# Kernel optimization log

Hardware: AMD Instinct MI355X
Metric: run time of the kernel (lower is better)

Reference implementation:

```python
import jax, jax.numpy as jnp
import numpy as np

N = 50000      # nodes
E = 512000     # directed edges (module assumes 2nd half is reverse of 1st half)
DIN = 128      # in_channels
EDIM = 128     # edge_dim (== in_channels, required by HypergraphConv branch)
H = 4          # heads
C = 32         # out_channels per head
EPS = 1e-5     # BatchNorm eps


def _segment_softmax(logits, seg, num):
    # PyG-style scatter softmax over segments (stable: subtract per-segment max)
    m = jax.ops.segment_max(logits, seg, num_segments=num)
    m = jnp.where(jnp.isfinite(m), m, 0.0)
    ex = jnp.exp(logits - m[seg])
    s = jax.ops.segment_sum(ex, seg, num_segments=num)
    return ex / (s[seg] + 1e-16)


def setup_inputs() -> dict:
    key = jax.random.key(0)
    ks = jax.random.split(key, 24)

    def lin(k, fin, fout):
        return (jax.random.normal(k, (fin, fout), jnp.float32) / np.sqrt(fin)).astype(jnp.float32)

    return {
        "x": jax.random.normal(ks[0], (N, DIN), jnp.float32),
        "edge_attr": jax.random.normal(ks[1], (E, EDIM), jnp.float32),
        # TransformerConv params
        "Wq": lin(ks[2], DIN, H * C), "bq": 0.01 * jax.random.normal(ks[3], (H * C,), jnp.float32),
        "Wk": lin(ks[4], DIN, H * C), "bk": 0.01 * jax.random.normal(ks[5], (H * C,), jnp.float32),
        "Wv": lin(ks[6], DIN, H * C), "bv": 0.01 * jax.random.normal(ks[7], (H * C,), jnp.float32),
        "We2": lin(ks[8], EDIM, H * C), "be2": 0.01 * jax.random.normal(ks[9], (H * C,), jnp.float32),
        "We3": lin(ks[10], EDIM, H * C), "be3": 0.01 * jax.random.normal(ks[11], (H * C,), jnp.float32),
        "Wcon": lin(ks[12], H * C, C),
        # BatchNorm1d params
        "bn_w": 1.0 + 0.01 * jax.random.normal(ks[13], (C,), jnp.float32),
        "bn_b": 0.01 * jax.random.normal(ks[14], (C,), jnp.float32),
        # HypergraphConv params (use_attention=False, heads=1)
        "Wh1": lin(ks[15], EDIM, C),
        "Wh2": lin(ks[16], DIN, C),
        "bh": jnp.zeros((C,), jnp.float32),
        # integer inputs
        "edge_index": jax.random.randint(ks[17], (2, E), 0, N, dtype=jnp.int32),
        "batch": jnp.zeros((N,), jnp.int32),
    }


def reference(x, edge_attr, Wq, bq, Wk, bk, Wv, bv, We2, be2, We3, be3, Wcon,
              bn_w, bn_b, Wh1, Wh2, bh, edge_index, batch):
    n = x.shape[0]
    e = edge_index.shape[1]
    src, dst = edge_index[0], edge_index[1]

    # ---- TransformerConv (edge-attention message passing) ----
    q = (x @ Wq + bq).reshape(n, H, C)
    k = (x @ Wk + bk).reshape(n, H, C)
    v = (x @ Wv + bv).reshape(n, H, C)
    ea2 = (edge_attr @ We2 + be2).reshape(e, H, C)
    ea3 = (edge_attr @ We3 + be3).reshape(e, H, C)
    qi, kj, vj = q[dst], k[src], v[src]          # gather per edge: [E,H,C]
    scale = 1.0 / np.sqrt(C)
    a1 = _segment_softmax((qi * kj).sum(-1) * scale, dst, n)    # [E,H]
    a2 = _segment_softmax((qi * ea2).sum(-1) * scale, dst, n)   # [E,H]
    msg = (vj * a1[..., None] + ea3 * a2[..., None]).reshape(e, H * C) @ Wcon  # [E,C]
    x_gat = jax.ops.segment_sum(msg, dst, num_segments=n)       # [N,C]

    # BatchNorm1d (training-mode batch stats, biased var) + exact GELU
    mu = x_gat.mean(0)
    var = ((x_gat - mu) ** 2).mean(0)
    x_gat = jax.nn.gelu(bn_w * (x_gat - mu) * jax.lax.rsqrt(var + EPS) + bn_b,
                        approximate=False)

    # ---- DHT dual hypergraph + HypergraphConv (no attention) ----
    e2 = e // 2
    ei = edge_index[:, :e2]           # first half of (bidirectional) edges
    ea = edge_attr[:e2]
    he_node = jnp.repeat(jnp.arange(e2, dtype=jnp.int32), 2)  # dual-node (edge) ids, [2*E2]
    he_edge = ei.T.reshape(-1)                                 # hyperedge (orig node) ids, [2*E2]

    xh = ea @ Wh1      # lin(edge_attr): [E2,C] (heads=1)
    attr = x @ Wh2     # lin2(x):        [N,C]

    ones = jnp.ones((2 * e2,), jnp.float32)
    deg_d = jax.ops.segment_sum(ones, he_node, num_segments=e2)   # D (== 2 per edge)
    Dinv = jnp.where(deg_d > 0, 1.0 / deg_d, 0.0)
    deg_b = jax.ops.segment_sum(ones, he_edge, num_segments=n)    # B (node degree)
    Binv = jnp.where(deg_b > 0, 1.0 / deg_b, 0.0)

    # propagate 1: dual-node -> hyperedge, norm B, then add hyperedge_attr
    o1 = jax.ops.segment_sum(Binv[he_edge][:, None] * xh[he_node],
                             he_edge, num_segments=n) + attr       # [N,C]
    # propagate 2 (flipped): hyperedge -> dual-node, norm D, add bias
    edge_attr2 = jax.ops.segment_sum(Dinv[he_node][:, None] * o1[he_edge],
                                     he_node, num_segments=e2) + bh  # [E2,C]

    return (x_gat, edge_attr2)
```

## Files before the change

kernel.cpp:

```cpp
#include <hip/hip_runtime.h>
#include <math.h>

#define NN 50000
#define NE 512000
#define NE2 256000
#define SCALE 0.17677669529663687f
#define EPSV 1e-5f
#define CHUNK 128000

#define OFF_Q      0UL
#define OFF_K      6400000UL
#define OFF_V      12800000UL
#define OFF_ATTR   0UL
#define OFF_O1     1600000UL
#define OFF_XGAT   3200000UL
#define OFF_O1ACC  4800000UL
#define OFF_DEGB   6400000UL
#define OFF_STATS  6450000UL
#define OFF_EX1    19200000UL
#define OFF_EX2    21248000UL
#define OFF_CC     23296000UL
#define OFF_S1     31488000UL
#define OFF_S2     31688000UL
#define OFF_XH     19200000UL
#define OFF_AGG    31888000UL
#define OFF_WBT    38288000UL
#define OFF_BIASB  38304384UL

typedef __attribute__((ext_vector_type(8))) short bf16x8;
typedef __attribute__((ext_vector_type(8))) unsigned short us8;
typedef __attribute__((ext_vector_type(4))) float f32x4;

__device__ __forceinline__ unsigned short f2bf(float f) {
    unsigned int u = __float_as_uint(f);
    unsigned int r = (u + 0x7FFFu + ((u >> 16) & 1u)) >> 16;
    return (unsigned short)r;
}
__device__ __forceinline__ float bf2f(unsigned short u) {
    return __uint_as_float(((unsigned int)u) << 16);
}

__global__ void pack_w(const float* __restrict__ We2, const float* __restrict__ be2,
                       const float* __restrict__ We3, const float* __restrict__ be3,
                       unsigned short* __restrict__ WbT, float* __restrict__ biasb) {
    const int idx = blockIdx.x * 256 + threadIdx.x;
    if (idx < 32768) {
        const int j = idx >> 7;
        const int k = idx & 127;
        const float w = (j < 128) ? We2[k * 128 + j] : We3[k * 128 + (j - 128)];
        WbT[idx] = f2bf(w);
    } else if (idx < 33024) {
        const int jj = idx - 32768;
        biasb[jj] = (jj < 128) ? be2[jj] : be3[jj - 128];
    }
}

__global__ __launch_bounds__(256)
void gemm_ea(const float* __restrict__ A, const unsigned short* __restrict__ WbT,
             const float* __restrict__ biasb, unsigned short* __restrict__ Cc, int half) {
    __shared__ unsigned short As[128 * 72];
    __shared__ unsigned short Bs[128 * 72];
    const int tid = threadIdx.x;
    const int wave = tid >> 6;
    const int lane = tid & 63;
    const int quad = lane >> 4;
    const int l16 = lane & 15;
    const int m0 = (wave & 1) * 64;
    const int n0 = (wave >> 1) * 64;
    const size_t r0 = (size_t)blockIdx.x * 128;

    f32x4 acc[4][4];
    #pragma unroll
    for (int i = 0; i < 4; i++)
        #pragma unroll
        for (int j = 0; j < 4; j++) acc[i][j] = (f32x4){0.f, 0.f, 0.f, 0.f};

    for (int kh = 0; kh < 2; kh++) {
        #pragma unroll
        for (int i = 0; i < 8; i++) {
            const int q = tid + 256 * i;
            const int row = q >> 4;
            const int c4 = q & 15;
            const float4 a4 = *(const float4*)(A + (r0 + row) * 128 + kh * 64 + c4 * 4);
            ushort4 b4;
            b4.x = f2bf(a4.x); b4.y = f2bf(a4.y); b4.z = f2bf(a4.z); b4.w = f2bf(a4.w);
            *(ushort4*)(&As[row * 72 + c4 * 4]) = b4;
        }
        {
            const int n = tid >> 1;
            const int koff = (tid & 1) * 32;
            const unsigned short* src = WbT + (size_t)(half * 128 + n) * 128 + kh * 64 + koff;
            #pragma unroll
            for (int u = 0; u < 4; u++) {
                *(us8*)(&Bs[n * 72 + koff + 8 * u]) = *(const us8*)(src + 8 * u);
            }
        }
        __syncthreads();
        #pragma unroll
        for (int kc = 0; kc < 64; kc += 32) {
            bf16x8 af[4], bf[4];
            #pragma unroll
            for (int i = 0; i < 4; i++)
                af[i] = *(const bf16x8*)(&As[(m0 + 16 * i + l16) * 72 + kc + quad * 8]);
            #pragma unroll
            for (int j = 0; j < 4; j++)
                bf[j] = *(const bf16x8*)(&Bs[(n0 + 16 * j + l16) * 72 + kc + quad * 8]);
            #pragma unroll
            for (int i = 0; i < 4; i++)
                #pragma unroll
                for (int j = 0; j < 4; j++)
                    acc[i][j] = __builtin_amdgcn_mfma_f32_16x16x32_bf16(af[i], bf[j], acc[i][j], 0, 0, 0);
        }
        __syncthreads();
    }
    #pragma unroll
    for (int j = 0; j < 4; j++) {
        const int col = n0 + 16 * j + l16;
        const float bcol = biasb[half * 128 + col];
        #pragma unroll
        for (int i = 0; i < 4; i++) {
            #pragma unroll
            for (int r = 0; r < 4; r++) {
                const int row = m0 + 16 * i + quad * 4 + r;
                Cc[(r0 + row) * 128 + col] = f2bf(acc[i][j][r] + bcol);
            }
        }
    }
}

__global__ void qkv_kernel(const float* __restrict__ x,
                           const float* __restrict__ Wq, const float* __restrict__ bq,
                           const float* __restrict__ Wk, const float* __restrict__ bk,
                           const float* __restrict__ Wv, const float* __restrict__ bv,
                           float* __restrict__ q, float* __restrict__ k, float* __restrict__ v) {
    __shared__ float xs[8 * 128];
    const int tid = threadIdx.x;
    const int j = tid & 127;
    const int g = tid >> 7;
    const size_t n0 = (size_t)blockIdx.x * 8;
    ((float4*)xs)[tid] = ((const float4*)(x + n0 * 128))[tid];
    __syncthreads();
    float aq[4] = {0,0,0,0}, ak[4] = {0,0,0,0}, av[4] = {0,0,0,0};
    #pragma unroll 4
    for (int d = 0; d < 128; d++) {
        const float wq = Wq[d*128 + j];
        const float wk = Wk[d*128 + j];
        const float wv = Wv[d*128 + j];
        #pragma unroll
        for (int r = 0; r < 4; r++) {
            const float xv = xs[(g + 2*r)*128 + d];
            aq[r] += xv * wq; ak[r] += xv * wk; av[r] += xv * wv;
        }
    }
    const float bqv = bq[j], bkv = bk[j], bvv = bv[j];
    #pragma unroll
    for (int r = 0; r < 4; r++) {
        const size_t n = n0 + g + 2*r;
        q[n*128 + j] = aq[r] + bqv;
        k[n*128 + j] = ak[r] + bkv;
        v[n*128 + j] = av[r] + bvv;
    }
}

__global__ void pass1(const int* __restrict__ eidx,
                      const float* __restrict__ q, const float* __restrict__ k,
                      const unsigned short* __restrict__ Cc, long e_base,
                      float* __restrict__ ex1, float* __restrict__ ex2,
                      float* __restrict__ s1, float* __restrict__ s2) {
    const size_t e = (size_t)e_base + blockIdx.x * 4 + (threadIdx.x >> 6);
    const int lane = threadIdx.x & 63;
    const int src = eidx[e];
    const int dst = eidx[NE + e];
    const float2 qv = ((const float2*)(q + (size_t)dst * 128))[lane];
    const float2 kv = ((const float2*)(k + (size_t)src * 128))[lane];
    const unsigned int cc = ((const unsigned int*)(Cc + (e - e_base) * 128))[lane];
    const float ea2a = bf2f((unsigned short)(cc & 0xFFFF));
    const float ea2b = bf2f((unsigned short)(cc >> 16));
    float p1 = qv.x * kv.x + qv.y * kv.y;
    float p2 = qv.x * ea2a + qv.y * ea2b;
    #pragma unroll
    for (int off = 8; off > 0; off >>= 1) {
        p1 += __shfl_down(p1, off, 16);
        p2 += __shfl_down(p2, off, 16);
    }
    if ((lane & 15) == 0) {
        const int h = lane >> 4;
        const float v1 = __expf(p1 * SCALE);
        const float v2 = __expf(p2 * SCALE);
        ex1[e * 4 + h] = v1;
        ex2[e * 4 + h] = v2;
        atomicAdd(&s1[(size_t)dst * 4 + h], v1);
        atomicAdd(&s2[(size_t)dst * 4 + h], v2);
    }
}

__global__ void pass2(const int* __restrict__ eidx,
                      const float* __restrict__ v,
                      const unsigned short* __restrict__ Cc, long e_base,
                      const float* __restrict__ ex1, const float* __restrict__ ex2,
                      const float* __restrict__ s1, const float* __restrict__ s2,
                      float* __restrict__ agg) {
    const size_t e = (size_t)e_base + blockIdx.x * 4 + (threadIdx.x >> 6);
    const int lane = threadIdx.x & 63;
    const int src = eidx[e];
    const int dst = eidx[NE + e];
    float a1l = 0.f, a2l = 0.f;
    if (lane < 4) {
        a1l = ex1[e * 4 + lane] / (s1[(size_t)dst * 4 + lane] + 1e-16f);
        a2l = ex2[e * 4 + lane] / (s2[(size_t)dst * 4 + lane] + 1e-16f);
    }
    const int h1 = lane >> 5;
    const int h2 = 2 + (lane >> 5);
    const float a1c1 = __shfl(a1l, h1), a1c2 = __shfl(a1l, h2);
    const float a2c1 = __shfl(a2l, h1), a2c2 = __shfl(a2l, h2);
    const float vv1 = v[(size_t)src * 128 + lane];
    const float vv2 = v[(size_t)src * 128 + lane + 64];
    const float e31 = bf2f(Cc[(e - e_base) * 128 + lane]);
    const float e32 = bf2f(Cc[(e - e_base) * 128 + lane + 64]);
    atomicAdd(&agg[(size_t)dst * 128 + lane],      a1c1 * vv1 + a2c1 * e31);
    atomicAdd(&agg[(size_t)dst * 128 + lane + 64], a1c2 * vv2 + a2c2 * e32);
}

__global__ void gemm_d128_o32(const float* __restrict__ A, const float* __restrict__ W,
                              float* __restrict__ out) {
    __shared__ float as[8 * 128];
    const int tid = threadIdx.x;
    const int p = tid & 31;
    const int mm = tid >> 5;
    const size_t m0 = (size_t)blockIdx.x * 8;
    ((float4*)as)[tid] = ((const float4*)(A + m0 * 128))[tid];
    __syncthreads();
    float c0 = 0.f, c1 = 0.f, c2 = 0.f, c3 = 0.f;
    const float4* as4 = (const float4*)as;
    #pragma unroll 8
    for (int i = 0; i < 32; i++) {
        const float4 a4 = as4[mm*32 + i];
        c0 += a4.x * W[(4*i+0)*32 + p];
        c1 += a4.y * W[(4*i+1)*32 + p];
        c2 += a4.z * W[(4*i+2)*32 + p];
        c3 += a4.w * W[(4*i+3)*32 + p];
    }
    out[(m0 + mm)*32 + p] = (c0 + c1) + (c2 + c3);
}

__global__ void bn_stats(const float* __restrict__ xg, float* __restrict__ stats) {
    __shared__ float ls[256], lss[256];
    const int tid = threadIdx.x;
    float s = 0.f, ss = 0.f;
    for (size_t i = (size_t)blockIdx.x*256 + tid; i < (size_t)NN*32; i += (size_t)gridDim.x*256) {
        const float val = xg[i];
        s += val; ss += val * val;
    }
    ls[tid] = s; lss[tid] = ss;
    __syncthreads();
    if (tid < 32) {
        float as_ = 0.f, ass = 0.f;
        #pragma unroll
        for (int w = 0; w < 8; w++) { as_ += ls[tid + 32*w]; ass += lss[tid + 32*w]; }
        atomicAdd(&stats[tid], as_);
        atomicAdd(&stats[32 + tid], ass);
    }
}

__global__ void bn_gelu(const float* __restrict__ xg, const float* __restrict__ stats,
                        const float* __restrict__ bnw, const float* __restrict__ bnb,
                        float* __restrict__ out) {
    const size_t i = (size_t)blockIdx.x * 256 + threadIdx.x;
    const int c = i & 31;
    const float mu = stats[c] * (1.0f / NN);
    const float var = stats[32 + c] * (1.0f / NN) - mu * mu;
    const float xn = bnw[c] * (xg[i] - mu) * rsqrtf(var + EPSV) + bnb[c];
    out[i] = 0.5f * xn * (1.0f + erff(xn * 0.70710678118654752f));
}

__global__ void hyper_scatter(const float* __restrict__ xh, const int* __restrict__ eidx,
                              float* __restrict__ o1acc, float* __restrict__ degb) {
    const int tid = threadIdx.x;
    const int c = tid & 31;
    const size_t i = (size_t)blockIdx.x * 8 + (tid >> 5);
    const int src = eidx[i];
    const int dst = eidx[NE + i];
    const float xv = xh[i*32 + c];
    atomicAdd(&o1acc[(size_t)src*32 + c], xv);
    atomicAdd(&o1acc[(size_t)dst*32 + c], xv);
    if (c == 0) {
        atomicAdd(&degb[src], 1.0f);
        atomicAdd(&degb[dst], 1.0f);
    }
}

__global__ void o1_finalize(const float* __restrict__ o1acc, const float* __restrict__ degb,
                            const float* __restrict__ attr, float* __restrict__ o1) {
    const size_t i = (size_t)blockIdx.x * 256 + threadIdx.x;
    const int n = (int)(i >> 5);
    const float d = degb[n];
    const float binv = d > 0.f ? 1.0f / d : 0.0f;
    o1[i] = o1acc[i] * binv + attr[i];
}

__global__ void edge_out(const float* __restrict__ o1, const int* __restrict__ eidx,
                         const float* __restrict__ bh, float* __restrict__ out2) {
    const size_t idx = (size_t)blockIdx.x * 256 + threadIdx.x;
    const size_t i = idx >> 5;
    const int c = (int)(idx & 31);
    const int src = eidx[i];
    const int dst = eidx[NE + i];
    out2[idx] = 0.5f * (o1[(size_t)src*32 + c] + o1[(size_t)dst*32 + c]) + bh[c];
}

extern "C" void kernel_launch(void* const* d_in, const int* in_sizes, int n_in,
                              void* d_out, int out_size, void* d_ws, size_t ws_size,
                              hipStream_t stream) {
    const float* x    = (const float*)d_in[0];
    const float* eatt = (const float*)d_in[1];
    const float* Wq   = (const float*)d_in[2];
    const float* bq   = (const float*)d_in[3];
    const float* Wk   = (const float*)d_in[4];
    const float* bk   = (const float*)d_in[5];
    const float* Wv   = (const float*)d_in[6];
    const float* bv   = (const float*)d_in[7];
    const float* We2  = (const float*)d_in[8];
    const float* be2  = (const float*)d_in[9];
    const float* We3  = (const float*)d_in[10];
    const float* be3  = (const float*)d_in[11];
    const float* Wcon = (const float*)d_in[12];
    const float* bnw  = (const float*)d_in[13];
    const float* bnb  = (const float*)d_in[14];
    const float* Wh1  = (const float*)d_in[15];
    const float* Wh2  = (const float*)d_in[16];
    const float* bh   = (const float*)d_in[17];
    const int*   eidx = (const int*)d_in[18];

    float* ws = (float*)d_ws;
    float* q     = ws + OFF_Q;
    float* k     = ws + OFF_K;
    float* v     = ws + OFF_V;
    float* ex1   = ws + OFF_EX1;
    float* ex2   = ws + OFF_EX2;
    unsigned short* Cc = (unsigned short*)(ws + OFF_CC);
    float* s1    = ws + OFF_S1;
    float* s2    = ws + OFF_S2;
    float* agg   = ws + OFF_AGG;
    unsigned short* WbT = (unsigned short*)(ws + OFF_WBT);
    float* biasb = ws + OFF_BIASB;
    float* attr  = ws + OFF_ATTR;
    float* o1    = ws + OFF_O1;
    float* xgat  = ws + OFF_XGAT;
    float* o1acc = ws + OFF_O1ACC;
    float* degb  = ws + OFF_DEGB;
    float* stats = ws + OFF_STATS;
    float* xh    = ws + OFF_XH;
    float* out0  = (float*)d_out;
    float* out1  = (float*)d_out + (size_t)NN * 32;

    hipMemsetAsync(ws + OFF_S1, 0, (38288000UL - OFF_S1) * sizeof(float), stream);

    pack_w<<<129, 256, 0, stream>>>(We2, be2, We3, be3, WbT, biasb);
    qkv_kernel<<<6250, 256, 0, stream>>>(x, Wq, bq, Wk, bk, Wv, bv, q, k, v);

    for (int c = 0; c < 4; c++) {
        const long eb = (long)c * CHUNK;
        gemm_ea<<<1000, 256, 0, stream>>>(eatt + (size_t)eb * 128, WbT, biasb, Cc, 0);
        pass1<<<32000, 256, 0, stream>>>(eidx, q, k, Cc, eb, ex1, ex2, s1, s2);
    }
    for (int c = 0; c < 4; c++) {
        const long eb = (long)c * CHUNK;
        gemm_ea<<<1000, 256, 0, stream>>>(eatt + (size_t)eb * 128, WbT, biasb, Cc, 1);
        pass2<<<32000, 256, 0, stream>>>(eidx, v, Cc, eb, ex1, ex2, s1, s2, agg);
    }

    hipMemsetAsync(ws + OFF_O1ACC, 0, (6450064UL - OFF_O1ACC) * sizeof(float), stream);

    gemm_d128_o32<<<6250, 256, 0, stream>>>(agg, Wcon, xgat);
    bn_stats<<<256, 256, 0, stream>>>(xgat, stats);
    bn_gelu<<<6250, 256, 0, stream>>>(xgat, stats, bnw, bnb, out0);

    gemm_d128_o32<<<32000, 256, 0, stream>>>(eatt, Wh1, xh);
    gemm_d128_o32<<<6250, 256, 0, stream>>>(x, Wh2, attr);
    hyper_scatter<<<32000, 256, 0, stream>>>(xh, eidx, o1acc, degb);
    o1_finalize<<<6250, 256, 0, stream>>>(o1acc, degb, attr, o1);
    edge_out<<<32000, 256, 0, stream>>>(o1, eidx, bh, out1);
}
```

Baseline: 1.291 ms.

## Replace atomic edge scatter with CSR gather and bf16 MFMA QKV projection

Builds a CSR (destination-sorted edge list) with a histogram, a single-block scan and an atomic scatter. Softmax normalisation and aggregation are then done per node as a gather, with no float atomics on s1/s2/agg. The QKV projection moves to a bf16 MFMA GEMM that writes a packed bf16 qkv buffer. The edge GEMM now computes both We2 and We3 in one pass over all edges instead of chunked halves. This trades atomic contention and the repeated edge_attr reads for CSR build overhead, an unsorted edge-list gather order, reduced precision in q/k/v, and a much larger workspace.

Measured after the change: 1.458 ms. 1.13x slower.

```diff
diff --git a/kernel.cpp b/kernel.cpp
--- a/kernel.cpp
+++ b/kernel.cpp
@@ -6,26 +6,29 @@
 #define NE2 256000
 #define SCALE 0.17677669529663687f
 #define EPSV 1e-5f
-#define CHUNK 128000
-
-#define OFF_Q      0UL
-#define OFF_K      6400000UL
-#define OFF_V      12800000UL
-#define OFF_ATTR   0UL
-#define OFF_O1     1600000UL
-#define OFF_XGAT   3200000UL
-#define OFF_O1ACC  4800000UL
-#define OFF_DEGB   6400000UL
-#define OFF_STATS  6450000UL
-#define OFF_EX1    19200000UL
-#define OFF_EX2    21248000UL
-#define OFF_CC     23296000UL
-#define OFF_S1     31488000UL
-#define OFF_S2     31688000UL
-#define OFF_XH     19200000UL
-#define OFF_AGG    31888000UL
-#define OFF_WBT    38288000UL
-#define OFF_BIASB  38304384UL
+
+#define OFF_QKV     0UL
+#define OFF_CC      9600000UL
+#define OFF_EX1     75136000UL
+#define OFF_EX2     77184000UL
+#define OFF_AGG     79232000UL
+#define OFF_XH      85632000UL
+#define OFF_ATTR    93824000UL
+#define OFF_O1      95424000UL
+#define OFF_XGAT    97024000UL
+#define OFF_WQKVT   98624000UL
+#define OFF_WE23T   98648576UL
+#define OFF_BQKV    98664960UL
+#define OFF_BE23    98665344UL
+#define OFF_ROWPTR  98665600UL
+#define OFF_CURSOR  98715604UL
+#define OFF_ELIST   98765604UL
+#define OFF_DCNT    99277604UL
+#define OFF_O1ACC   99327604UL
+#define OFF_DEGB    100927604UL
+#define OFF_STATS   100977604UL
+#define ZERO_START  OFF_DCNT
+#define ZERO_END    100977668UL
 
 typedef __attribute__((ext_vector_type(8))) short bf16x8;
 typedef __attribute__((ext_vector_type(8))) unsigned short us8;
@@ -40,26 +43,32 @@
     return __uint_as_float(((unsigned int)u) << 16);
 }
 
-__global__ void pack_w(const float* __restrict__ We2, const float* __restrict__ be2,
-                       const float* __restrict__ We3, const float* __restrict__ be3,
-                       unsigned short* __restrict__ WbT, float* __restrict__ biasb) {
+__global__ void pack_wt(const float* __restrict__ W, unsigned short* __restrict__ Bt) {
     const int idx = blockIdx.x * 256 + threadIdx.x;
-    if (idx < 32768) {
-        const int j = idx >> 7;
-        const int k = idx & 127;
-        const float w = (j < 128) ? We2[k * 128 + j] : We3[k * 128 + (j - 128)];
-        WbT[idx] = f2bf(w);
-    } else if (idx < 33024) {
-        const int jj = idx - 32768;
-        biasb[jj] = (jj < 128) ? be2[jj] : be3[jj - 128];
+    const int j = idx >> 7;
+    const int k = idx & 127;
+    Bt[idx] = f2bf(W[k * 128 + j]);
+}
+
+__global__ void bias_pack(const float* __restrict__ bq, const float* __restrict__ bk,
+                          const float* __restrict__ bv, const float* __restrict__ be2,
+                          const float* __restrict__ be3, float* __restrict__ BQKV,
+                          float* __restrict__ BE23) {
+    const int idx = blockIdx.x * 256 + threadIdx.x;
+    if (idx < 384) {
+        BQKV[idx] = (idx < 128) ? bq[idx] : (idx < 256 ? bk[idx - 128] : bv[idx - 256]);
+    } else if (idx < 640) {
+        const int j = idx - 384;
+        BE23[j] = (j < 128) ? be2[j] : be3[j - 128];
     }
 }
 
 __global__ __launch_bounds__(256)
-void gemm_ea(const float* __restrict__ A, const unsigned short* __restrict__ WbT,
-             const float* __restrict__ biasb, unsigned short* __restrict__ Cc, int half) {
-    __shared__ unsigned short As[128 * 72];
-    __shared__ unsigned short Bs[128 * 72];
+void gemm_node(const float* __restrict__ A, const unsigned short* __restrict__ Bt,
+               const float* __restrict__ bias, unsigned short* __restrict__ out,
+               int M, int Ntot) {
+    __shared__ unsigned short As[2][128 * 72];
+    __shared__ unsigned short Bs[2][128 * 72];
     const int tid = threadIdx.x;
     const int wave = tid >> 6;
     const int lane = tid & 63;
@@ -69,115 +78,89 @@
     const int n0 = (wave >> 1) * 64;
     const size_t r0 = (size_t)blockIdx.x * 128;
 
-    f32x4 acc[4][4];
     #pragma unroll
-    for (int i = 0; i < 4; i++)
-        #pragma unroll
-        for (int j = 0; j < 4; j++) acc[i][j] = (f32x4){0.f, 0.f, 0.f, 0.f};
-
     for (int kh = 0; kh < 2; kh++) {
         #pragma unroll
         for (int i = 0; i < 8; i++) {
             const int q = tid + 256 * i;
             const int row = q >> 4;
             const int c4 = q & 15;
-            const float4 a4 = *(const float4*)(A + (r0 + row) * 128 + kh * 64 + c4 * 4);
+            const long gr = (long)r0 + row;
+            float4 a4 = {0.f, 0.f, 0.f, 0.f};
+            if (gr < M) a4 = *(const float4*)(A + gr * 128 + kh * 64 + c4 * 4);
             ushort4 b4;
             b4.x = f2bf(a4.x); b4.y = f2bf(a4.y); b4.z = f2bf(a4.z); b4.w = f2bf(a4.w);
-            *(ushort4*)(&As[row * 72 + c4 * 4]) = b4;
+            *(ushort4*)(&As[kh][row * 72 + c4 * 4]) = b4;
         }
-        {
+    }
+    const int nslab = Ntot >> 7;
+    for (int s = 0; s < nslab; s++) {
+        __syncthreads();
+        #pragma unroll
+        for (int kh = 0; kh < 2; kh++) {
             const int n = tid >> 1;
             const int koff = (tid & 1) * 32;
-            const unsigned short* src = WbT + (size_t)(half * 128 + n) * 128 + kh * 64 + koff;
+            const unsigned short* src = Bt + (size_t)(s * 128 + n) * 128 + kh * 64 + koff;
             #pragma unroll
-            for (int u = 0; u < 4; u++) {
-                *(us8*)(&Bs[n * 72 + koff + 8 * u]) = *(const us8*)(src + 8 * u);
+            for (int u = 0; u < 4; u++)
+                *(us8*)(&Bs[kh][n * 72 + koff + 8 * u]) = *(const us8*)(src + 8 * u);
+        }
+        __syncthreads();
+        f32x4 acc[4][4];
+        #pragma unroll
+        for (int i = 0; i < 4; i++)
+            #pragma unroll
+            for (int j = 0; j < 4; j++) acc[i][j] = (f32x4){0.f, 0.f, 0.f, 0.f};
+        #pragma unroll
+        for (int kh = 0; kh < 2; kh++) {
+            #pragma unroll
+            for (int kc = 0; kc < 64; kc += 32) {
+                bf16x8 af[4], bfr[4];
+                #pragma unroll
+                for (int i = 0; i < 4; i++)
+                    af[i] = *(const bf16x8*)(&As[kh][(m0 + 16 * i + l16) * 72 + kc + quad * 8]);
+                #pragma unroll
+                for (int j = 0; j < 4; j++)
+                    bfr[j] = *(const bf16x8*)(&Bs[kh][(n0 + 16 * j + l16) * 72 + kc + quad * 8]);
+                #pragma unroll
+                for (int i = 0; i < 4; i++)
+                    #pragma unroll
+                    for (int j = 0; j < 4; j++)
+                        acc[i][j] = __builtin_amdgcn_mfma_f32_16x16x32_bf16(af[i], bfr[j], acc[i][j], 0, 0, 0);
             }
         }
-        __syncthreads();
-        #pragma unroll
-        for (int kc = 0; kc < 64; kc += 32) {
-            bf16x8 af[4], bf[4];
+        #pragma unroll
+        for (int j = 0; j < 4; j++) {
+            const int col = n0 + 16 * j + l16;
+            const float bcol = bias[s * 128 + col];
             #pragma unroll
-            for (int i = 0; i < 4; i++)
-                af[i] = *(const bf16x8*)(&As[(m0 + 16 * i + l16) * 72 + kc + quad * 8]);
-            #pragma unroll
-            for (int j = 0; j < 4; j++)
-                bf[j] = *(const bf16x8*)(&Bs[(n0 + 16 * j + l16) * 72 + kc + quad * 8]);
-            #pragma unroll
-            for (int i = 0; i < 4; i++)
+            for (int i = 0; i < 4; i++) {
                 #pragma unroll
-                for (int j = 0; j < 4; j++)
-                    acc[i][j] = __builtin_amdgcn_mfma_f32_16x16x32_bf16(af[i], bf[j], acc[i][j], 0, 0, 0);
-        }
-        __syncthreads();
-    }
-    #pragma unroll
-    for (int j = 0; j < 4; j++) {
-        const int col = n0 + 16 * j + l16;
-        const float bcol = biasb[half * 128 + col];
-        #pragma unroll
-        for (int i = 0; i < 4; i++) {
-            #pragma unroll
-            for (int r = 0; r < 4; r++) {
-                const int row = m0 + 16 * i + quad * 4 + r;
-                Cc[(r0 + row) * 128 + col] = f2bf(acc[i][j][r] + bcol);
+                for (int r = 0; r < 4; r++) {
+                    const long row = (long)r0 + m0 + 16 * i + quad * 4 + r;
+                    if (row < M)
+                        out[row * Ntot + s * 128 + col] = f2bf(acc[i][j][r] + bcol);
+                }
             }
         }
     }
 }
 
-__global__ void qkv_kernel(const float* __restrict__ x,
-                           const float* __restrict__ Wq, const float* __restrict__ bq,
-                           const float* __restrict__ Wk, const float* __restrict__ bk,
-                           const float* __restrict__ Wv, const float* __restrict__ bv,
-                           float* __restrict__ q, float* __restrict__ k, float* __restrict__ v) {
-    __shared__ float xs[8 * 128];
-    const int tid = threadIdx.x;
-    const int j = tid & 127;
-    const int g = tid >> 7;
-    const size_t n0 = (size_t)blockIdx.x * 8;
-    ((float4*)xs)[tid] = ((const float4*)(x + n0 * 128))[tid];
-    __syncthreads();
-    float aq[4] = {0,0,0,0}, ak[4] = {0,0,0,0}, av[4] = {0,0,0,0};
-    #pragma unroll 4
-    for (int d = 0; d < 128; d++) {
-        const float wq = Wq[d*128 + j];
-        const float wk = Wk[d*128 + j];
-        const float wv = Wv[d*128 + j];
-        #pragma unroll
-        for (int r = 0; r < 4; r++) {
-            const float xv = xs[(g + 2*r)*128 + d];
-            aq[r] += xv * wq; ak[r] += xv * wk; av[r] += xv * wv;
-        }
-    }
-    const float bqv = bq[j], bkv = bk[j], bvv = bv[j];
-    #pragma unroll
-    for (int r = 0; r < 4; r++) {
-        const size_t n = n0 + g + 2*r;
-        q[n*128 + j] = aq[r] + bqv;
-        k[n*128 + j] = ak[r] + bkv;
-        v[n*128 + j] = av[r] + bvv;
-    }
-}
-
-__global__ void pass1(const int* __restrict__ eidx,
-                      const float* __restrict__ q, const float* __restrict__ k,
-                      const unsigned short* __restrict__ Cc, long e_base,
-                      float* __restrict__ ex1, float* __restrict__ ex2,
-                      float* __restrict__ s1, float* __restrict__ s2) {
-    const size_t e = (size_t)e_base + blockIdx.x * 4 + (threadIdx.x >> 6);
+__global__ void pass1(const int* __restrict__ eidx, const unsigned short* __restrict__ qkv,
+                      const unsigned short* __restrict__ Cc,
+                      float* __restrict__ ex1, float* __restrict__ ex2) {
+    const size_t e = (size_t)blockIdx.x * 4 + (threadIdx.x >> 6);
     const int lane = threadIdx.x & 63;
     const int src = eidx[e];
     const int dst = eidx[NE + e];
-    const float2 qv = ((const float2*)(q + (size_t)dst * 128))[lane];
-    const float2 kv = ((const float2*)(k + (size_t)src * 128))[lane];
-    const unsigned int cc = ((const unsigned int*)(Cc + (e - e_base) * 128))[lane];
-    const float ea2a = bf2f((unsigned short)(cc & 0xFFFF));
-    const float ea2b = bf2f((unsigned short)(cc >> 16));
-    float p1 = qv.x * kv.x + qv.y * kv.y;
-    float p2 = qv.x * ea2a + qv.y * ea2b;
+    const unsigned int qp = *(const unsigned int*)(qkv + (size_t)dst * 384 + 2 * lane);
+    const unsigned int kp = *(const unsigned int*)(qkv + (size_t)src * 384 + 128 + 2 * lane);
+    const unsigned int ep = *(const unsigned int*)(Cc + (size_t)e * 256 + 2 * lane);
+    const float qx = bf2f((unsigned short)(qp & 0xFFFF)), qy = bf2f((unsigned short)(qp >> 16));
+    const float kx = bf2f((unsigned short)(kp & 0xFFFF)), ky = bf2f((unsigned short)(kp >> 16));
+    const float e2x = bf2f((unsigned short)(ep & 0xFFFF)), e2y = bf2f((unsigned short)(ep >> 16));
+    float p1 = qx * kx + qy * ky;
+    float p2 = qx * e2x + qy * e2y;
     #pragma unroll
     for (int off = 8; off > 0; off >>= 1) {
         p1 += __shfl_down(p1, off, 16);
@@ -185,40 +168,85 @@
     }
     if ((lane & 15) == 0) {
         const int h = lane >> 4;
-        const float v1 = __expf(p1 * SCALE);
-        const float v2 = __expf(p2 * SCALE);
-        ex1[e * 4 + h] = v1;
-        ex2[e * 4 + h] = v2;
-        atomicAdd(&s1[(size_t)dst * 4 + h], v1);
-        atomicAdd(&s2[(size_t)dst * 4 + h], v2);
-    }
-}
-
-__global__ void pass2(const int* __restrict__ eidx,
-                      const float* __restrict__ v,
-                      const unsigned short* __restrict__ Cc, long e_base,
-                      const float* __restrict__ ex1, const float* __restrict__ ex2,
-                      const float* __restrict__ s1, const float* __restrict__ s2,
-                      float* __restrict__ agg) {
-    const size_t e = (size_t)e_base + blockIdx.x * 4 + (threadIdx.x >> 6);
+        ex1[e * 4 + h] = __expf(p1 * SCALE);
+        ex2[e * 4 + h] = __expf(p2 * SCALE);
+    }
+}
+
+__global__ void csr_hist(const int* __restrict__ eidx, int* __restrict__ dcnt) {
+    const int e = blockIdx.x * 256 + threadIdx.x;
+    atomicAdd(&dcnt[eidx[NE + e]], 1);
+}
+
+__global__ __launch_bounds__(1024)
+void scan50k(const int* __restrict__ dcnt, int* __restrict__ rowptr, int* __restrict__ cursor) {
+    __shared__ int part[1024];
+    const int t = threadIdx.x;
+    const int per = 49;
+    const int base = t * per;
+    int s = 0;
+    for (int i = 0; i < per; i++) {
+        const int n = base + i;
+        if (n < NN) s += dcnt[n];
+    }
+    part[t] = s;
+    __syncthreads();
+    for (int off = 1; off < 1024; off <<= 1) {
+        const int vv = (t >= off) ? part[t - off] : 0;
+        __syncthreads();
+        part[t] += vv;
+        __syncthreads();
+    }
+    int run = (t == 0) ? 0 : part[t - 1];
+    for (int i = 0; i < per; i++) {
+        const int n = base + i;
+        if (n < NN) {
+            rowptr[n] = run;
+            cursor[n] = run;
+            run += dcnt[n];
+        }
+    }
+    if (base <= NN - 1 && NN - 1 < base + per) rowptr[NN] = run;
+}
+
+__global__ void csr_scatter(const int* __restrict__ eidx, int* __restrict__ cursor,
+                            int* __restrict__ elist) {
+    const int e = blockIdx.x * 256 + threadIdx.x;
+    const int dst = eidx[NE + e];
+    const int pos = atomicAdd(&cursor[dst], 1);
+    elist[pos] = e;
+}
+
+__global__ void pass2_gather(const int* __restrict__ eidx, const int* __restrict__ rowptr,
+                             const int* __restrict__ elist,
+                             const unsigned short* __restrict__ qkv,
+                             const unsigned short* __restrict__ Cc,
+                             const float* __restrict__ ex1, const float* __restrict__ ex2,
+                             float* __restrict__ agg) {
+    const int n = blockIdx.x * 4 + (threadIdx.x >> 6);
     const int lane = threadIdx.x & 63;
-    const int src = eidx[e];
-    const int dst = eidx[NE + e];
-    float a1l = 0.f, a2l = 0.f;
-    if (lane < 4) {
-        a1l = ex1[e * 4 + lane] / (s1[(size_t)dst * 4 + lane] + 1e-16f);
-        a2l = ex2[e * 4 + lane] / (s2[(size_t)dst * 4 + lane] + 1e-16f);
-    }
-    const int h1 = lane >> 5;
-    const int h2 = 2 + (lane >> 5);
-    const float a1c1 = __shfl(a1l, h1), a1c2 = __shfl(a1l, h2);
-    const float a2c1 = __shfl(a2l, h1), a2c2 = __shfl(a2l, h2);
-    const float vv1 = v[(size_t)src * 128 + lane];
-    const float vv2 = v[(size_t)src * 128 + lane + 64];
-    const float e31 = bf2f(Cc[(e - e_base) * 128 + lane]);
-    const float e32 = bf2f(Cc[(e - e_base) * 128 + lane + 64]);
-    atomicAdd(&agg[(size_t)dst * 128 + lane],      a1c1 * vv1 + a2c1 * e31);
-    atomicAdd(&agg[(size_t)dst * 128 + lane + 64], a1c2 * vv2 + a2c2 * e32);
+    const int h = lane >> 4;
+    const int beg = rowptr[n], end = rowptr[n + 1];
+    float s1 = 0.f, s2 = 0.f;
+    for (int i = beg; i < end; i++) {
+        const int e = elist[i];
+        s1 += ex1[(size_t)e * 4 + h];
+        s2 += ex2[(size_t)e * 4 + h];
+    }
+    const float r1 = 1.f / (s1 + 1e-16f);
+    const float r2 = 1.f / (s2 + 1e-16f);
+    float ax = 0.f, ay = 0.f;
+    for (int i = beg; i < end; i++) {
+        const int e = elist[i];
+        const int src = eidx[e];
+        const float w1 = ex1[(size_t)e * 4 + h] * r1;
+        const float w2 = ex2[(size_t)e * 4 + h] * r2;
+        const unsigned int vp = *(const unsigned int*)(qkv + (size_t)src * 384 + 256 + 2 * lane);
+        const unsigned int e3 = *(const unsigned int*)(Cc + (size_t)e * 256 + 128 + 2 * lane);
+        ax += w1 * bf2f((unsigned short)(vp & 0xFFFF)) + w2 * bf2f((unsigned short)(e3 & 0xFFFF));
+        ay += w1 * bf2f((unsigned short)(vp >> 16)) + w2 * bf2f((unsigned short)(e3 >> 16));
+    }
+    *(float2*)(agg + (size_t)n * 128 + 2 * lane) = make_float2(ax, ay);
 }
 
 __global__ void gemm_d128_o32(const float* __restrict__ A, const float* __restrict__ W,
@@ -332,44 +360,47 @@
     const int*   eidx = (const int*)d_in[18];
 
     float* ws = (float*)d_ws;
-    float* q     = ws + OFF_Q;
-    float* k     = ws + OFF_K;
-    float* v     = ws + OFF_V;
+    unsigned short* qkv   = (unsigned short*)(ws + OFF_QKV);
+    unsigned short* Cc    = (unsigned short*)(ws + OFF_CC);
     float* ex1   = ws + OFF_EX1;
     float* ex2   = ws + OFF_EX2;
-    unsigned short* Cc = (unsigned short*)(ws + OFF_CC);
-    float* s1    = ws + OFF_S1;
-    float* s2    = ws + OFF_S2;
     float* agg   = ws + OFF_AGG;
-    unsigned short* WbT = (unsigned short*)(ws + OFF_WBT);
-    float* biasb = ws + OFF_BIASB;
+    float* xh    = ws + OFF_XH;
     float* attr  = ws + OFF_ATTR;
     float* o1    = ws + OFF_O1;
     float* xgat  = ws + OFF_XGAT;
+    unsigned short* WQKVT = (unsigned short*)(ws + OFF_WQKVT);
+    unsigned short* WE23T = (unsigned short*)(ws + OFF_WE23T);
+    float* BQKV  = ws + OFF_BQKV;
+    float* BE23  = ws + OFF_BE23;
+    int* rowptr  = (int*)(ws + OFF_ROWPTR);
+    int* cursor  = (int*)(ws + OFF_CURSOR);
+    int* elist   = (int*)(ws + OFF_ELIST);
+    int* dcnt    = (int*)(ws + OFF_DCNT);
     float* o1acc = ws + OFF_O1ACC;
     float* degb  = ws + OFF_DEGB;
     float* stats = ws + OFF_STATS;
-    float* xh    = ws + OFF_XH;
     float* out0  = (float*)d_out;
     float* out1  = (float*)d_out + (size_t)NN * 32;
 
-    hipMemsetAsync(ws + OFF_S1, 0, (38288000UL - OFF_S1) * sizeof(float), stream);
-
-    pack_w<<<129, 256, 0, stream>>>(We2, be2, We3, be3, WbT, biasb);
-    qkv_kernel<<<6250, 256, 0, stream>>>(x, Wq, bq, Wk, bk, Wv, bv, q, k, v);
-
-    for (int c = 0; c < 4; c++) {
-        const long eb = (long)c * CHUNK;
-        gemm_ea<<<1000, 256, 0, stream>>>(eatt + (size_t)eb * 128, WbT, biasb, Cc, 0);
-        pass1<<<32000, 256, 0, stream>>>(eidx, q, k, Cc, eb, ex1, ex2, s1, s2);
-    }
-    for (int c = 0; c < 4; c++) {
-        const long eb = (long)c * CHUNK;
-        gemm_ea<<<1000, 256, 0, stream>>>(eatt + (size_t)eb * 128, WbT, biasb, Cc, 1);
-        pass2<<<32000, 256, 0, stream>>>(eidx, v, Cc, eb, ex1, ex2, s1, s2, agg);
-    }
-
-    hipMemsetAsync(ws + OFF_O1ACC, 0, (6450064UL - OFF_O1ACC) * sizeof(float), stream);
+    hipMemsetAsync(ws + ZERO_START, 0, (ZERO_END - ZERO_START) * sizeof(float), stream);
+
+    pack_wt<<<64, 256, 0, stream>>>(Wq, WQKVT);
+    pack_wt<<<64, 256, 0, stream>>>(Wk, WQKVT + 128 * 128);
+    pack_wt<<<64, 256, 0, stream>>>(Wv, WQKVT + 256 * 128);
+    pack_wt<<<64, 256, 0, stream>>>(We2, WE23T);
+    pack_wt<<<64, 256, 0, stream>>>(We3, WE23T + 128 * 128);
+    bias_pack<<<3, 256, 0, stream>>>(bq, bk, bv, be2, be3, BQKV, BE23);
+
+    csr_hist<<<2000, 256, 0, stream>>>(eidx, dcnt);
+    scan50k<<<1, 1024, 0, stream>>>(dcnt, rowptr, cursor);
+    csr_scatter<<<2000, 256, 0, stream>>>(eidx, cursor, elist);
+
+    gemm_node<<<391, 256, 0, stream>>>(x, WQKVT, BQKV, qkv, NN, 384);
+    gemm_node<<<4000, 256, 0, stream>>>(eatt, WE23T, BE23, Cc, NE, 256);
+
+    pass1<<<128000, 256, 0, stream>>>(eidx, qkv, Cc, ex1, ex2);
+    pass2_gather<<<12500, 256, 0, stream>>>(eidx, rowptr, elist, qkv, Cc, ex1, ex2, agg);
 
     gemm_d128_o32<<<6250, 256, 0, stream>>>(agg, Wcon, xgat);
     bn_stats<<<256, 256, 0, stream>>>(xgat, stats);
```
